# Kernel optimization log

Hardware: AMD Instinct MI355X
Metric: run time of the kernel (lower is better)

The kernel has to match this reference:

```python
import jax, jax.numpy as jnp
import numpy as np

P, M_DIM, R_DIM = 1024, 64, 32


def setup_inputs() -> dict:
    key = jax.random.key(0)
    k1, k2, k3, k4, k5 = jax.random.split(key, 5)
    hidden_state = jax.random.normal(k1, (P, M_DIM), dtype=jnp.float32)
    corr_index = jax.random.normal(k2, (P, P, 2), dtype=jnp.float32)
    nei_index = jax.random.randint(k3, (P, P), 0, 2, dtype=jnp.int32)
    # params: rela_embed Linear(2, r_dim); attention Linear(2*m_dim + r_dim, 1)
    # init_weights_attr: normal(mean=0, std=0.2), bias 0
    W_rela = 0.2 * jax.random.normal(k4, (2, R_DIM), dtype=jnp.float32)
    b_rela = jnp.zeros((R_DIM,), dtype=jnp.float32)
    W_att = 0.2 * jax.random.normal(k5, (2 * M_DIM + R_DIM, 1), dtype=jnp.float32)
    b_att = jnp.zeros((1,), dtype=jnp.float32)
    return {
        "hidden_state": hidden_state,
        "corr_index": corr_index,
        "nei_index": nei_index,
        "W_rela": W_rela,
        "b_rela": b_rela,
        "W_att": W_att,
        "b_att": b_att,
    }


def reference(hidden_state, corr_index, nei_index, W_rela, b_rela, W_att, b_att):
    m = hidden_state.shape[1]
    r = W_rela.shape[1]
    mask = nei_index > 0  # [P, P]; entry (i, j): j is a neighbor of i

    # rela_embed -> relu (dropout is identity at eval time)
    rela = jax.nn.relu(jnp.einsum('ijc,cr->ijr', corr_index, W_rela) + b_rela)  # [P,P,r]

    # attention Linear over cat([rela, h_i, h_j]); decompose the weight so we
    # never materialize the [P,P, r+2m] concatenation.
    w = W_att[:, 0]
    w_r, w_hi, w_nei = w[:r], w[r:r + m], w[r + m:]
    scores = (jnp.einsum('ijr,r->ij', rela, w_r)
              + (hidden_state @ w_hi)[:, None]
              + (hidden_state @ w_nei)[None, :]
              + b_att[0])  # [P,P]

    # masked-out entries get 0, then every exact zero becomes -1e-6 (as in source)
    Pos = jnp.where(mask, scores, 0.0)
    Pos = jnp.where(Pos == 0.0, -1e-6, Pos)
    Pos = jax.nn.softmax(Pos, axis=1)

    # weighted scatter-sum: H[i,j] = mask * Pos[i,j] * h_j ; sum over j
    social_tensor = jnp.einsum('ij,jm->im', Pos * mask.astype(Pos.dtype), hidden_state)
    return social_tensor
```

## Files before the change

kernel.cpp:

```cpp
#include <hip/hip_runtime.h>

#define PP   1024
#define MM   64
#define RR   32
#define ROWS 4
#define TPB  512
#define NW   (TPB / 64)
#define JPT  (PP / TPB)

__global__ __launch_bounds__(256) void proj_kernel(
    const float* __restrict__ hidden,
    const float* __restrict__ W_att,
    const float* __restrict__ b_att,
    float* __restrict__ ws)
{
    const int wid  = threadIdx.x >> 6;
    const int lane = threadIdx.x & 63;
    const int p = blockIdx.x * 4 + wid;

    float h = hidden[p * MM + lane];
    float a = h * W_att[RR + lane];
    float b = h * W_att[RR + MM + lane];
#pragma unroll
    for (int off = 32; off > 0; off >>= 1) {
        a += __shfl_down(a, off, 64);
        b += __shfl_down(b, off, 64);
    }
    if (lane == 0) {
        ws[p]      = a + b_att[0];
        ws[PP + p] = b;
    }
}

__global__ __launch_bounds__(TPB, 2) void social_kernel(
    const float* __restrict__ hidden,
    const float* __restrict__ corr,
    const int*   __restrict__ nei,
    const float* __restrict__ W_rela,
    const float* __restrict__ b_rela,
    const float* __restrict__ W_att,
    const float* __restrict__ ws,
    float* __restrict__ out)
{
    __shared__ float4 q4[PP];
    __shared__ float4 red[NW];
    __shared__ float  partf[NW][ROWS][MM];

    const int t    = threadIdx.x;
    const int lane = t & 63;
    const int wid  = t >> 6;
    const int i0   = blockIdx.x * ROWS;

    float4 W0[RR / 4], W1[RR / 4], Bv[RR / 4], Wr[RR / 4];
    {
        const float4* W_rela4 = (const float4*)W_rela;
        const float4* b4      = (const float4*)b_rela;
        const float4* wa4     = (const float4*)W_att;
#pragma unroll
        for (int k = 0; k < RR / 4; ++k) {
            W0[k] = W_rela4[k];
            W1[k] = W_rela4[RR / 4 + k];
            Bv[k] = b4[k];
            Wr[k] = wa4[k];
        }
    }
    float hib[ROWS];
#pragma unroll
    for (int r = 0; r < ROWS; ++r) hib[r] = ws[i0 + r];

    float posv[JPT][ROWS];
    float mskv[JPT][ROWS];
#pragma unroll
    for (int jj = 0; jj < JPT; ++jj) {
        const int j = t + jj * TPB;
        const float hn = ws[PP + j];
#pragma unroll
        for (int r = 0; r < ROWS; ++r) {
            const int row = i0 + r;
            const float2 c = ((const float2*)corr)[row * PP + j];
            const int nv = nei[row * PP + j];
            float s = 0.f;
#pragma unroll
            for (int k = 0; k < RR / 4; ++k) {
                float t0 = fmaxf(fmaf(c.x, W0[k].x, fmaf(c.y, W1[k].x, Bv[k].x)), 0.f);
                float t1 = fmaxf(fmaf(c.x, W0[k].y, fmaf(c.y, W1[k].y, Bv[k].y)), 0.f);
                float t2 = fmaxf(fmaf(c.x, W0[k].z, fmaf(c.y, W1[k].z, Bv[k].z)), 0.f);
                float t3 = fmaxf(fmaf(c.x, W0[k].w, fmaf(c.y, W1[k].w, Bv[k].w)), 0.f);
                s = fmaf(t0, Wr[k].x, s);
                s = fmaf(t1, Wr[k].y, s);
                s = fmaf(t2, Wr[k].z, s);
                s = fmaf(t3, Wr[k].w, s);
            }
            const float score = s + hib[r] + hn;
            float pos = (nv > 0) ? score : 0.0f;
            pos = (pos == 0.0f) ? -1e-6f : pos;
            posv[jj][r] = pos;
            mskv[jj][r] = (nv > 0) ? 1.0f : 0.0f;
        }
    }

    float m4[ROWS];
#pragma unroll
    for (int r = 0; r < ROWS; ++r) {
        float m = posv[0][r];
#pragma unroll
        for (int jj = 1; jj < JPT; ++jj) m = fmaxf(m, posv[jj][r]);
        m4[r] = m;
    }
#pragma unroll
    for (int off = 32; off > 0; off >>= 1) {
#pragma unroll
        for (int r = 0; r < ROWS; ++r)
            m4[r] = fmaxf(m4[r], __shfl_xor(m4[r], off, 64));
    }
    if (lane == 0) red[wid] = make_float4(m4[0], m4[1], m4[2], m4[3]);
    __syncthreads();
#pragma unroll
    for (int w = 0; w < NW; ++w) {
        const float4 v = red[w];
        m4[0] = fmaxf(m4[0], v.x);
        m4[1] = fmaxf(m4[1], v.y);
        m4[2] = fmaxf(m4[2], v.z);
        m4[3] = fmaxf(m4[3], v.w);
    }

    float e[JPT][ROWS];
    float s4[ROWS] = {0.f, 0.f, 0.f, 0.f};
#pragma unroll
    for (int jj = 0; jj < JPT; ++jj) {
#pragma unroll
        for (int r = 0; r < ROWS; ++r) {
            const float ev = __expf(posv[jj][r] - m4[r]);
            e[jj][r] = ev;
            s4[r] += ev;
        }
    }
#pragma unroll
    for (int off = 32; off > 0; off >>= 1) {
#pragma unroll
        for (int r = 0; r < ROWS; ++r)
            s4[r] += __shfl_xor(s4[r], off, 64);
    }
    __syncthreads();
    if (lane == 0) red[wid] = make_float4(s4[0], s4[1], s4[2], s4[3]);
    __syncthreads();
    {
        float a0 = 0.f, a1 = 0.f, a2 = 0.f, a3 = 0.f;
#pragma unroll
        for (int w = 0; w < NW; ++w) {
            const float4 v = red[w];
            a0 += v.x; a1 += v.y; a2 += v.z; a3 += v.w;
        }
        s4[0] = a0; s4[1] = a1; s4[2] = a2; s4[3] = a3;
    }
    float inv[ROWS];
#pragma unroll
    for (int r = 0; r < ROWS; ++r) inv[r] = 1.0f / s4[r];

#pragma unroll
    for (int jj = 0; jj < JPT; ++jj) {
        const int j = t + jj * TPB;
        q4[j] = make_float4(e[jj][0] * mskv[jj][0] * inv[0],
                            e[jj][1] * mskv[jj][1] * inv[1],
                            e[jj][2] * mskv[jj][2] * inv[2],
                            e[jj][3] * mskv[jj][3] * inv[3]);
    }
    __syncthreads();

    const int m = lane;
    const int g = wid;
    float acc[ROWS] = {0.f, 0.f, 0.f, 0.f};
#pragma unroll 4
    for (int j = g; j < PP; j += NW) {
        const float4 q = q4[j];
        const float h = hidden[j * MM + m];
        acc[0] = fmaf(q.x, h, acc[0]);
        acc[1] = fmaf(q.y, h, acc[1]);
        acc[2] = fmaf(q.z, h, acc[2]);
        acc[3] = fmaf(q.w, h, acc[3]);
    }
#pragma unroll
    for (int r = 0; r < ROWS; ++r) partf[g][r][m] = acc[r];
    __syncthreads();

    if (t < ROWS * MM) {
        const int row = t >> 6;
        const int col = t & 63;
        float s = 0.f;
#pragma unroll
        for (int w = 0; w < NW; ++w) s += partf[w][row][col];
        out[(i0 + row) * MM + col] = s;
    }
}

extern "C" void kernel_launch(void* const* d_in, const int* in_sizes, int n_in,
                              void* d_out, int out_size, void* d_ws, size_t ws_size,
                              hipStream_t stream)
{
    const float* hidden = (const float*)d_in[0];
    const float* corr   = (const float*)d_in[1];
    const int*   nei    = (const int*)d_in[2];
    const float* W_rela = (const float*)d_in[3];
    const float* b_rela = (const float*)d_in[4];
    const float* W_att  = (const float*)d_in[5];
    const float* b_att  = (const float*)d_in[6];
    float* ws  = (float*)d_ws;
    float* out = (float*)d_out;

    proj_kernel<<<PP / 4, 256, 0, stream>>>(hidden, W_att, b_att, ws);
    social_kernel<<<PP / ROWS, TPB, 0, stream>>>(hidden, corr, nei, W_rela,
                                                 b_rela, W_att, ws, out);
}
```

Baseline: 90.15 us.

## Use 1024-thread blocks with one column per thread and float4 weighted-sum loop

Doubles the block size so each thread handles a single neighbor column, removing the per-thread j loop in the score and softmax phases. The weighted aggregation is restructured so each lane loads a float4 slice of hidden and processes four j rows per wave, with an xor-shuffle reduction across lane groups. This is meant to raise memory-level parallelism and widen global loads. In exchange, the larger block means heavier __syncthreads barriers, a 16-wave final reduction, and more register pressure under the new launch bound.

```diff
diff --git a/kernel.cpp b/kernel.cpp
--- a/kernel.cpp
+++ b/kernel.cpp
@@ -4,9 +4,8 @@
 #define MM   64
 #define RR   32
 #define ROWS 4
-#define TPB  512
+#define TPB  1024
 #define NW   (TPB / 64)
-#define JPT  (PP / TPB)
 
 __global__ __launch_bounds__(256) void proj_kernel(
     const float* __restrict__ hidden,
@@ -32,7 +31,7 @@
     }
 }
 
-__global__ __launch_bounds__(TPB, 2) void social_kernel(
+__global__ __launch_bounds__(TPB, 4) void social_kernel(
     const float* __restrict__ hidden,
     const float* __restrict__ corr,
     const int*   __restrict__ nei,
@@ -68,45 +67,42 @@
 #pragma unroll
     for (int r = 0; r < ROWS; ++r) hib[r] = ws[i0 + r];
 
-    float posv[JPT][ROWS];
-    float mskv[JPT][ROWS];
-#pragma unroll
-    for (int jj = 0; jj < JPT; ++jj) {
-        const int j = t + jj * TPB;
-        const float hn = ws[PP + j];
-#pragma unroll
-        for (int r = 0; r < ROWS; ++r) {
-            const int row = i0 + r;
-            const float2 c = ((const float2*)corr)[row * PP + j];
-            const int nv = nei[row * PP + j];
-            float s = 0.f;
-#pragma unroll
-            for (int k = 0; k < RR / 4; ++k) {
-                float t0 = fmaxf(fmaf(c.x, W0[k].x, fmaf(c.y, W1[k].x, Bv[k].x)), 0.f);
-                float t1 = fmaxf(fmaf(c.x, W0[k].y, fmaf(c.y, W1[k].y, Bv[k].y)), 0.f);
-                float t2 = fmaxf(fmaf(c.x, W0[k].z, fmaf(c.y, W1[k].z, Bv[k].z)), 0.f);
-                float t3 = fmaxf(fmaf(c.x, W0[k].w, fmaf(c.y, W1[k].w, Bv[k].w)), 0.f);
-                s = fmaf(t0, Wr[k].x, s);
-                s = fmaf(t1, Wr[k].y, s);
-                s = fmaf(t2, Wr[k].z, s);
-                s = fmaf(t3, Wr[k].w, s);
-            }
-            const float score = s + hib[r] + hn;
-            float pos = (nv > 0) ? score : 0.0f;
-            pos = (pos == 0.0f) ? -1e-6f : pos;
-            posv[jj][r] = pos;
-            mskv[jj][r] = (nv > 0) ? 1.0f : 0.0f;
-        }
+    const int j = t;
+    const float hn = ws[PP + j];
+
+    float2 c[ROWS];
+    int    nv[ROWS];
+#pragma unroll
+    for (int r = 0; r < ROWS; ++r) {
+        c[r]  = ((const float2*)corr)[(i0 + r) * PP + j];
+        nv[r] = nei[(i0 + r) * PP + j];
+    }
+
+    float pos[ROWS], msk[ROWS];
+#pragma unroll
+    for (int r = 0; r < ROWS; ++r) {
+        float s = 0.f;
+#pragma unroll
+        for (int k = 0; k < RR / 4; ++k) {
+            float t0 = fmaxf(fmaf(c[r].x, W0[k].x, fmaf(c[r].y, W1[k].x, Bv[k].x)), 0.f);
+            float t1 = fmaxf(fmaf(c[r].x, W0[k].y, fmaf(c[r].y, W1[k].y, Bv[k].y)), 0.f);
+            float t2 = fmaxf(fmaf(c[r].x, W0[k].z, fmaf(c[r].y, W1[k].z, Bv[k].z)), 0.f);
+            float t3 = fmaxf(fmaf(c[r].x, W0[k].w, fmaf(c[r].y, W1[k].w, Bv[k].w)), 0.f);
+            s = fmaf(t0, Wr[k].x, s);
+            s = fmaf(t1, Wr[k].y, s);
+            s = fmaf(t2, Wr[k].z, s);
+            s = fmaf(t3, Wr[k].w, s);
+        }
+        const float score = s + hib[r] + hn;
+        float p = (nv[r] > 0) ? score : 0.0f;
+        p = (p == 0.0f) ? -1e-6f : p;
+        pos[r] = p;
+        msk[r] = (nv[r] > 0) ? 1.0f : 0.0f;
     }
 
     float m4[ROWS];
 #pragma unroll
-    for (int r = 0; r < ROWS; ++r) {
-        float m = posv[0][r];
-#pragma unroll
-        for (int jj = 1; jj < JPT; ++jj) m = fmaxf(m, posv[jj][r]);
-        m4[r] = m;
-    }
+    for (int r = 0; r < ROWS; ++r) m4[r] = pos[r];
 #pragma unroll
     for (int off = 32; off > 0; off >>= 1) {
 #pragma unroll
@@ -124,16 +120,11 @@
         m4[3] = fmaxf(m4[3], v.w);
     }
 
-    float e[JPT][ROWS];
-    float s4[ROWS] = {0.f, 0.f, 0.f, 0.f};
-#pragma unroll
-    for (int jj = 0; jj < JPT; ++jj) {
-#pragma unroll
-        for (int r = 0; r < ROWS; ++r) {
-            const float ev = __expf(posv[jj][r] - m4[r]);
-            e[jj][r] = ev;
-            s4[r] += ev;
-        }
+    float e4[ROWS], s4[ROWS];
+#pragma unroll
+    for (int r = 0; r < ROWS; ++r) {
+        e4[r] = __expf(pos[r] - m4[r]);
+        s4[r] = e4[r];
     }
 #pragma unroll
     for (int off = 32; off > 0; off >>= 1) {
@@ -153,34 +144,57 @@
         }
         s4[0] = a0; s4[1] = a1; s4[2] = a2; s4[3] = a3;
     }
-    float inv[ROWS];
-#pragma unroll
-    for (int r = 0; r < ROWS; ++r) inv[r] = 1.0f / s4[r];
-
-#pragma unroll
-    for (int jj = 0; jj < JPT; ++jj) {
-        const int j = t + jj * TPB;
-        q4[j] = make_float4(e[jj][0] * mskv[jj][0] * inv[0],
-                            e[jj][1] * mskv[jj][1] * inv[1],
-                            e[jj][2] * mskv[jj][2] * inv[2],
-                            e[jj][3] * mskv[jj][3] * inv[3]);
-    }
-    __syncthreads();
-
-    const int m = lane;
-    const int g = wid;
-    float acc[ROWS] = {0.f, 0.f, 0.f, 0.f};
+
+    q4[j] = make_float4(e4[0] * msk[0] / s4[0],
+                        e4[1] * msk[1] / s4[1],
+                        e4[2] * msk[2] / s4[2],
+                        e4[3] * msk[3] / s4[3]);
+    __syncthreads();
+
+    const int q_idx = lane >> 4;
+    const int mslot = lane & 15;
+    float4 acc[ROWS];
+#pragma unroll
+    for (int r = 0; r < ROWS; ++r) acc[r] = make_float4(0.f, 0.f, 0.f, 0.f);
+
 #pragma unroll 4
-    for (int j = g; j < PP; j += NW) {
-        const float4 q = q4[j];
-        const float h = hidden[j * MM + m];
-        acc[0] = fmaf(q.x, h, acc[0]);
-        acc[1] = fmaf(q.y, h, acc[1]);
-        acc[2] = fmaf(q.z, h, acc[2]);
-        acc[3] = fmaf(q.w, h, acc[3]);
-    }
-#pragma unroll
-    for (int r = 0; r < ROWS; ++r) partf[g][r][m] = acc[r];
+    for (int it = 0; it < 16; ++it) {
+        const int jj = wid * 4 + q_idx + it * 64;
+        const float4 h4 = ((const float4*)hidden)[jj * (MM / 4) + mslot];
+        const float4 q  = q4[jj];
+        acc[0].x = fmaf(q.x, h4.x, acc[0].x);
+        acc[0].y = fmaf(q.x, h4.y, acc[0].y);
+        acc[0].z = fmaf(q.x, h4.z, acc[0].z);
+        acc[0].w = fmaf(q.x, h4.w, acc[0].w);
+        acc[1].x = fmaf(q.y, h4.x, acc[1].x);
+        acc[1].y = fmaf(q.y, h4.y, acc[1].y);
+        acc[1].z = fmaf(q.y, h4.z, acc[1].z);
+        acc[1].w = fmaf(q.y, h4.w, acc[1].w);
+        acc[2].x = fmaf(q.z, h4.x, acc[2].x);
+        acc[2].y = fmaf(q.z, h4.y, acc[2].y);
+        acc[2].z = fmaf(q.z, h4.z, acc[2].z);
+        acc[2].w = fmaf(q.z, h4.w, acc[2].w);
+        acc[3].x = fmaf(q.w, h4.x, acc[3].x);
+        acc[3].y = fmaf(q.w, h4.y, acc[3].y);
+        acc[3].z = fmaf(q.w, h4.z, acc[3].z);
+        acc[3].w = fmaf(q.w, h4.w, acc[3].w);
+    }
+
+#pragma unroll
+    for (int off = 16; off <= 32; off <<= 1) {
+#pragma unroll
+        for (int r = 0; r < ROWS; ++r) {
+            acc[r].x += __shfl_xor(acc[r].x, off, 64);
+            acc[r].y += __shfl_xor(acc[r].y, off, 64);
+            acc[r].z += __shfl_xor(acc[r].z, off, 64);
+            acc[r].w += __shfl_xor(acc[r].w, off, 64);
+        }
+    }
+    if (lane < 16) {
+#pragma unroll
+        for (int r = 0; r < ROWS; ++r)
+            ((float4*)&partf[wid][r][0])[mslot] = acc[r];
+    }
     __syncthreads();
 
     if (t < ROWS * MM) {
```

New measurement: 86.87 us. -3.6%, faster.
